# Optimization experiments

Hardware: AMD Instinct MI355X
Metric: run time of the kernel (lower is better)

Reference implementation:

```python
import jax, jax.numpy as jnp
import numpy as np

OBS_DIM = 256
ACTION_DIM = 4
NUM_OBJECTS = 16
HIDDEN = 512
BATCH = 4096
LN_EPS = 1e-5


def _uniform(key, shape, stdv):
    return jax.random.uniform(key, shape, jnp.float32, -stdv, stdv)


def setup_inputs() -> dict:
    key = jax.random.key(0)
    ks = jax.random.split(key, 8)
    node_in = OBS_DIM + ACTION_DIM
    s1 = 1.0 / np.sqrt(HIDDEN)
    s3 = 1.0 / np.sqrt(OBS_DIM)
    return {
        "states": jax.random.normal(ks[0], (BATCH, NUM_OBJECTS, OBS_DIM), jnp.float32),
        "action": jax.random.randint(ks[1], (BATCH,), 0, ACTION_DIM * NUM_OBJECTS, jnp.int64 if jax.config.jax_enable_x64 else jnp.int32),
        "W1": _uniform(ks[2], (node_in, HIDDEN), s1),
        "b1": _uniform(ks[3], (HIDDEN,), s1),
        "W2": _uniform(ks[4], (HIDDEN, HIDDEN), s1),
        "b2": _uniform(ks[5], (HIDDEN,), s1),
        "W3": _uniform(ks[6], (HIDDEN, OBS_DIM), s3),
        "b3": _uniform(ks[7], (OBS_DIM,), s3),
        "ln_g": jnp.ones((HIDDEN,), jnp.float32),
        "ln_b": jnp.zeros((HIDDEN,), jnp.float32),
    }


def _gc(x, W, b):
    # x: [B, O, d_in]. adj = block_diag(ones(O,O)/O) == per-graph mean pooling,
    # broadcast back to every node in the graph.
    s = jnp.einsum("bod,dh->boh", x, W)
    m = jnp.mean(s, axis=1, keepdims=True)  # [B, 1, h]
    return jnp.broadcast_to(m, s.shape) + b


def _layernorm(x, g, b):
    mu = jnp.mean(x, axis=-1, keepdims=True)
    var = jnp.mean(jnp.square(x - mu), axis=-1, keepdims=True)
    return (x - mu) * jax.lax.rsqrt(var + LN_EPS) * g + b


def reference(states, action, W1, b1, W2, b2, W3, b3, ln_g, ln_b):
    B, O, D = states.shape
    # one_hot(action, A*O).view(-1, A) == per-node one-hot slices
    a = jax.nn.one_hot(action, ACTION_DIM * O, dtype=states.dtype)
    a = a.reshape(B, O, ACTION_DIM)
    x = jnp.concatenate([states, a], axis=-1)  # [B, O, D+A]
    h = jax.nn.relu(_gc(x, W1, b1))
    h = jax.nn.relu(_layernorm(_gc(h, W2, b2), ln_g, ln_b))
    out = _gc(h, W3, b3)  # [B, O, obs_dim]
    return out
```

## Files before the change

kernel.cpp:

```cpp
#include <hip/hip_runtime.h>
#include <hip/hip_bf16.h>

#define BSZ   4096
#define NOBJ  16
#define DOBS  256
#define ADIM  4
#define HID   512
#define KP1   288

#define MB    16
#define XP1   296
#define HP    520
#define TP    260

typedef unsigned short u16;
typedef __bf16 bf16x8 __attribute__((ext_vector_type(8)));
typedef float  f32x4  __attribute__((ext_vector_type(4)));
typedef unsigned short u16x8 __attribute__((ext_vector_type(8)));

static __device__ __forceinline__ u16 f2bf(float f) {
    __hip_bfloat16 h = __float2bfloat16(f);
    return __builtin_bit_cast(u16, h);
}
static __device__ __forceinline__ bf16x8 ldg8(const u16* p) {
    return __builtin_bit_cast(bf16x8, *(const u16x8*)p);
}

__global__ void prep_weights(const float* __restrict__ W1, const float* __restrict__ W2,
                             const float* __restrict__ W3,
                             u16* __restrict__ W1T, u16* __restrict__ W2T, u16* __restrict__ W3T) {
    int idx = blockIdx.x * 256 + threadIdx.x;
    const int n1 = HID * KP1;
    const int n2 = HID * HID;
    const int n3 = DOBS * HID;
    if (idx < n1) {
        int h = idx / KP1, k = idx % KP1;
        float v = (k < DOBS + ADIM) ? W1[k * HID + h] : 0.0f;
        W1T[idx] = f2bf(v);
    } else if (idx < n1 + n2) {
        int t = idx - n1;
        int h = t / HID, k = t % HID;
        W2T[t] = f2bf(W2[k * HID + h]);
    } else if (idx < n1 + n2 + n3) {
        int t = idx - n1 - n2;
        int n = t / HID, k = t % HID;
        W3T[t] = f2bf(W3[k * DOBS + n]);
    }
}

__global__ __launch_bounds__(256) void fused_mlp(
    const float* __restrict__ states, const int* __restrict__ action,
    const u16* __restrict__ W1T, const float* __restrict__ b1,
    const u16* __restrict__ W2T, const float* __restrict__ b2,
    const u16* __restrict__ W3T, const float* __restrict__ b3,
    const float* __restrict__ lng, const float* __restrict__ lnb,
    float* __restrict__ out)
{
    __shared__ u16   xbar[MB][XP1];
    __shared__ u16   h1[MB][HP];
    __shared__ u16   h2[MB][HP];
    __shared__ float t3[MB][TP];
    __shared__ float red[2][4][MB];

    const int t  = threadIdx.x;
    const int w  = t >> 6;
    const int l  = t & 63;
    const int lr = l & 15;
    const int lg = l >> 4;
    const int b0 = blockIdx.x * MB;

    {
        const int d = t;
        #pragma unroll 4
        for (int r = 0; r < MB; ++r) {
            const float* sp = states + ((size_t)(b0 + r) * NOBJ) * DOBS + d;
            float s = 0.f;
            #pragma unroll
            for (int o = 0; o < NOBJ; ++o) s += sp[o * DOBS];
            xbar[r][d] = f2bf(s * (1.0f / NOBJ));
        }
        if (t < MB) {
            int a = action[b0 + t] & 3;
            #pragma unroll
            for (int k = 0; k < KP1 - DOBS; ++k)
                xbar[t][DOBS + k] = f2bf(k == a ? (1.0f / NOBJ) : 0.0f);
        }
    }
    __syncthreads();

    {
        f32x4 acc[8] = {};
        #pragma unroll 3
        for (int ks = 0; ks < KP1 / 32; ++ks) {
            bf16x8 a = ldg8(&xbar[lr][ks * 32 + lg * 8]);
            #pragma unroll
            for (int nb = 0; nb < 8; ++nb) {
                int n = w * 128 + nb * 16 + lr;
                bf16x8 bv = ldg8(W1T + (size_t)n * KP1 + ks * 32 + lg * 8);
                acc[nb] = __builtin_amdgcn_mfma_f32_16x16x32_bf16(a, bv, acc[nb], 0, 0, 0);
            }
        }
        #pragma unroll
        for (int nb = 0; nb < 8; ++nb) {
            int n = w * 128 + nb * 16 + lr;
            float bias = b1[n];
            #pragma unroll
            for (int r = 0; r < 4; ++r)
                h1[lg * 4 + r][n] = f2bf(fmaxf(acc[nb][r] + bias, 0.f));
        }
    }
    __syncthreads();

    {
        f32x4 acc[8] = {};
        #pragma unroll 4
        for (int ks = 0; ks < HID / 32; ++ks) {
            bf16x8 a = ldg8(&h1[lr][ks * 32 + lg * 8]);
            #pragma unroll
            for (int nb = 0; nb < 8; ++nb) {
                int n = w * 128 + nb * 16 + lr;
                bf16x8 bv = ldg8(W2T + (size_t)n * HID + ks * 32 + lg * 8);
                acc[nb] = __builtin_amdgcn_mfma_f32_16x16x32_bf16(a, bv, acc[nb], 0, 0, 0);
            }
        }
        float s1[4] = {0.f, 0.f, 0.f, 0.f}, s2[4] = {0.f, 0.f, 0.f, 0.f};
        #pragma unroll
        for (int nb = 0; nb < 8; ++nb) {
            float bias = b2[w * 128 + nb * 16 + lr];
            #pragma unroll
            for (int r = 0; r < 4; ++r) {
                float v = acc[nb][r] + bias;
                acc[nb][r] = v;
                s1[r] += v;
                s2[r] += v * v;
            }
        }
        #pragma unroll
        for (int r = 0; r < 4; ++r) {
            #pragma unroll
            for (int m = 8; m; m >>= 1) {
                s1[r] += __shfl_xor(s1[r], m, 64);
                s2[r] += __shfl_xor(s2[r], m, 64);
            }
            if (lr == 0) {
                red[0][w][lg * 4 + r] = s1[r];
                red[1][w][lg * 4 + r] = s2[r];
            }
        }
        __syncthreads();
        float muv[4], rsv[4];
        #pragma unroll
        for (int r = 0; r < 4; ++r) {
            int m = lg * 4 + r;
            float S1 = red[0][0][m] + red[0][1][m] + red[0][2][m] + red[0][3][m];
            float S2 = red[1][0][m] + red[1][1][m] + red[1][2][m] + red[1][3][m];
            float mu = S1 * (1.0f / HID);
            float var = S2 * (1.0f / HID) - mu * mu;
            muv[r] = mu;
            rsv[r] = rsqrtf(var + 1e-5f);
        }
        #pragma unroll
        for (int nb = 0; nb < 8; ++nb) {
            int n = w * 128 + nb * 16 + lr;
            float g = lng[n], bb = lnb[n];
            #pragma unroll
            for (int r = 0; r < 4; ++r) {
                float y = (acc[nb][r] - muv[r]) * rsv[r] * g + bb;
                h2[lg * 4 + r][n] = f2bf(fmaxf(y, 0.f));
            }
        }
    }
    __syncthreads();

    {
        f32x4 acc[4] = {};
        #pragma unroll 4
        for (int ks = 0; ks < HID / 32; ++ks) {
            bf16x8 a = ldg8(&h2[lr][ks * 32 + lg * 8]);
            #pragma unroll
            for (int nb = 0; nb < 4; ++nb) {
                int n = w * 64 + nb * 16 + lr;
                bf16x8 bv = ldg8(W3T + (size_t)n * HID + ks * 32 + lg * 8);
                acc[nb] = __builtin_amdgcn_mfma_f32_16x16x32_bf16(a, bv, acc[nb], 0, 0, 0);
            }
        }
        #pragma unroll
        for (int nb = 0; nb < 4; ++nb) {
            int n = w * 64 + nb * 16 + lr;
            float bias = b3[n];
            #pragma unroll
            for (int r = 0; r < 4; ++r)
                t3[lg * 4 + r][n] = acc[nb][r] + bias;
        }
    }
    __syncthreads();

    {
        #pragma unroll 4
        for (int i = 0; i < 64; ++i) {
            int flat = i * 256 + t;
            int d4 = flat & 63;
            int o  = (flat >> 6) & 15;
            int r  = flat >> 10;
            float4 v = *(const float4*)&t3[r][d4 * 4];
            *(float4*)(out + ((size_t)(b0 + r) * NOBJ + o) * DOBS + d4 * 4) = v;
        }
    }
}

extern "C" void kernel_launch(void* const* d_in, const int* in_sizes, int n_in,
                              void* d_out, int out_size, void* d_ws, size_t ws_size,
                              hipStream_t stream) {
    const float* states = (const float*)d_in[0];
    const int*   action = (const int*)d_in[1];
    const float* W1 = (const float*)d_in[2];
    const float* b1 = (const float*)d_in[3];
    const float* W2 = (const float*)d_in[4];
    const float* b2 = (const float*)d_in[5];
    const float* W3 = (const float*)d_in[6];
    const float* b3 = (const float*)d_in[7];
    const float* lng = (const float*)d_in[8];
    const float* lnb = (const float*)d_in[9];
    float* out = (float*)d_out;

    char* ws = (char*)d_ws;
    size_t off = 0;
    auto alloc = [&](size_t bytes) -> void* {
        void* p = ws + off;
        off = (off + bytes + 255) & ~(size_t)255;
        return p;
    };
    u16* W1T = (u16*)alloc((size_t)HID * KP1 * 2);
    u16* W2T = (u16*)alloc((size_t)HID * HID * 2);
    u16* W3T = (u16*)alloc((size_t)DOBS * HID * 2);

    prep_weights<<<2112, 256, 0, stream>>>(W1, W2, W3, W1T, W2T, W3T);
    fused_mlp<<<BSZ / MB, 256, 0, stream>>>(states, action,
                                            W1T, b1, W2T, b2, W3T, b3,
                                            lng, lnb, out);
}
```

Baseline: 161.3 us.

## Double block to 512 threads and vectorize states mean-pooling loads

Raises the fused kernel's block from 4 to 8 waves, so each wave computes half as many output columns in every GEMM stage and the LayerNorm reduction sums across 8 waves. The states mean pooling now uses float4 loads and writes four bf16 values at once. The aim is more parallelism and memory-level concurrency per block for the load-bound pooling and store phases, at the cost of larger blocks, which may lower the number of resident blocks per CU.

```diff
diff --git a/kernel.cpp b/kernel.cpp
--- a/kernel.cpp
+++ b/kernel.cpp
@@ -9,6 +9,7 @@
 #define KP1   288
 
 #define MB    16
+#define NT    512
 #define XP1   296
 #define HP    520
 #define TP    260
@@ -17,6 +18,7 @@
 typedef __bf16 bf16x8 __attribute__((ext_vector_type(8)));
 typedef float  f32x4  __attribute__((ext_vector_type(4)));
 typedef unsigned short u16x8 __attribute__((ext_vector_type(8)));
+typedef unsigned short u16x4 __attribute__((ext_vector_type(4)));
 
 static __device__ __forceinline__ u16 f2bf(float f) {
     __hip_bfloat16 h = __float2bfloat16(f);
@@ -48,7 +50,7 @@
     }
 }
 
-__global__ __launch_bounds__(256) void fused_mlp(
+__global__ __launch_bounds__(NT) void fused_mlp(
     const float* __restrict__ states, const int* __restrict__ action,
     const u16* __restrict__ W1T, const float* __restrict__ b1,
     const u16* __restrict__ W2T, const float* __restrict__ b2,
@@ -60,7 +62,7 @@
     __shared__ u16   h1[MB][HP];
     __shared__ u16   h2[MB][HP];
     __shared__ float t3[MB][TP];
-    __shared__ float red[2][4][MB];
+    __shared__ float red[2][8][MB];
 
     const int t  = threadIdx.x;
     const int w  = t >> 6;
@@ -70,14 +72,21 @@
     const int b0 = blockIdx.x * MB;
 
     {
-        const int d = t;
-        #pragma unroll 4
-        for (int r = 0; r < MB; ++r) {
-            const float* sp = states + ((size_t)(b0 + r) * NOBJ) * DOBS + d;
-            float s = 0.f;
-            #pragma unroll
-            for (int o = 0; o < NOBJ; ++o) s += sp[o * DOBS];
-            xbar[r][d] = f2bf(s * (1.0f / NOBJ));
+        const float4* sf4 = (const float4*)states;
+        #pragma unroll
+        for (int p = 0; p < 2; ++p) {
+            int idx = p * NT + t;
+            int r = idx >> 6, d4 = idx & 63;
+            float sx = 0.f, sy = 0.f, sz = 0.f, sw = 0.f;
+            const float4* rp = sf4 + (((size_t)(b0 + r) * NOBJ) << 6) + d4;
+            #pragma unroll
+            for (int o = 0; o < NOBJ; ++o) {
+                float4 v = rp[o << 6];
+                sx += v.x; sy += v.y; sz += v.z; sw += v.w;
+            }
+            u16x4 st = { f2bf(sx * (1.0f / NOBJ)), f2bf(sy * (1.0f / NOBJ)),
+                         f2bf(sz * (1.0f / NOBJ)), f2bf(sw * (1.0f / NOBJ)) };
+            *(u16x4*)&xbar[r][d4 * 4] = st;
         }
         if (t < MB) {
             int a = action[b0 + t] & 3;
@@ -89,20 +98,20 @@
     __syncthreads();
 
     {
-        f32x4 acc[8] = {};
+        f32x4 acc[4] = {};
         #pragma unroll 3
         for (int ks = 0; ks < KP1 / 32; ++ks) {
             bf16x8 a = ldg8(&xbar[lr][ks * 32 + lg * 8]);
             #pragma unroll
-            for (int nb = 0; nb < 8; ++nb) {
-                int n = w * 128 + nb * 16 + lr;
+            for (int nb = 0; nb < 4; ++nb) {
+                int n = w * 64 + nb * 16 + lr;
                 bf16x8 bv = ldg8(W1T + (size_t)n * KP1 + ks * 32 + lg * 8);
                 acc[nb] = __builtin_amdgcn_mfma_f32_16x16x32_bf16(a, bv, acc[nb], 0, 0, 0);
             }
         }
         #pragma unroll
-        for (int nb = 0; nb < 8; ++nb) {
-            int n = w * 128 + nb * 16 + lr;
+        for (int nb = 0; nb < 4; ++nb) {
+            int n = w * 64 + nb * 16 + lr;
             float bias = b1[n];
             #pragma unroll
             for (int r = 0; r < 4; ++r)
@@ -112,21 +121,21 @@
     __syncthreads();
 
     {
-        f32x4 acc[8] = {};
+        f32x4 acc[4] = {};
         #pragma unroll 4
         for (int ks = 0; ks < HID / 32; ++ks) {
             bf16x8 a = ldg8(&h1[lr][ks * 32 + lg * 8]);
             #pragma unroll
-            for (int nb = 0; nb < 8; ++nb) {
-                int n = w * 128 + nb * 16 + lr;
+            for (int nb = 0; nb < 4; ++nb) {
+                int n = w * 64 + nb * 16 + lr;
                 bf16x8 bv = ldg8(W2T + (size_t)n * HID + ks * 32 + lg * 8);
                 acc[nb] = __builtin_amdgcn_mfma_f32_16x16x32_bf16(a, bv, acc[nb], 0, 0, 0);
             }
         }
         float s1[4] = {0.f, 0.f, 0.f, 0.f}, s2[4] = {0.f, 0.f, 0.f, 0.f};
         #pragma unroll
-        for (int nb = 0; nb < 8; ++nb) {
-            float bias = b2[w * 128 + nb * 16 + lr];
+        for (int nb = 0; nb < 4; ++nb) {
+            float bias = b2[w * 64 + nb * 16 + lr];
             #pragma unroll
             for (int r = 0; r < 4; ++r) {
                 float v = acc[nb][r] + bias;
@@ -152,16 +161,17 @@
         #pragma unroll
         for (int r = 0; r < 4; ++r) {
             int m = lg * 4 + r;
-            float S1 = red[0][0][m] + red[0][1][m] + red[0][2][m] + red[0][3][m];
-            float S2 = red[1][0][m] + red[1][1][m] + red[1][2][m] + red[1][3][m];
+            float S1 = 0.f, S2 = 0.f;
+            #pragma unroll
+            for (int ww = 0; ww < 8; ++ww) { S1 += red[0][ww][m]; S2 += red[1][ww][m]; }
             float mu = S1 * (1.0f / HID);
             float var = S2 * (1.0f / HID) - mu * mu;
             muv[r] = mu;
             rsv[r] = rsqrtf(var + 1e-5f);
         }
         #pragma unroll
-        for (int nb = 0; nb < 8; ++nb) {
-            int n = w * 128 + nb * 16 + lr;
+        for (int nb = 0; nb < 4; ++nb) {
+            int n = w * 64 + nb * 16 + lr;
             float g = lng[n], bb = lnb[n];
             #pragma unroll
             for (int r = 0; r < 4; ++r) {
@@ -173,20 +183,20 @@
     __syncthreads();
 
     {
-        f32x4 acc[4] = {};
+        f32x4 acc[2] = {};
         #pragma unroll 4
         for (int ks = 0; ks < HID / 32; ++ks) {
             bf16x8 a = ldg8(&h2[lr][ks * 32 + lg * 8]);
             #pragma unroll
-            for (int nb = 0; nb < 4; ++nb) {
-                int n = w * 64 + nb * 16 + lr;
+            for (int nb = 0; nb < 2; ++nb) {
+                int n = w * 32 + nb * 16 + lr;
                 bf16x8 bv = ldg8(W3T + (size_t)n * HID + ks * 32 + lg * 8);
                 acc[nb] = __builtin_amdgcn_mfma_f32_16x16x32_bf16(a, bv, acc[nb], 0, 0, 0);
             }
         }
         #pragma unroll
-        for (int nb = 0; nb < 4; ++nb) {
-            int n = w * 64 + nb * 16 + lr;
+        for (int nb = 0; nb < 2; ++nb) {
+            int n = w * 32 + nb * 16 + lr;
             float bias = b3[n];
             #pragma unroll
             for (int r = 0; r < 4; ++r)
@@ -196,9 +206,9 @@
     __syncthreads();
 
     {
-        #pragma unroll 4
-        for (int i = 0; i < 64; ++i) {
-            int flat = i * 256 + t;
+        #pragma unroll 8
+        for (int i = 0; i < 32; ++i) {
+            int flat = i * NT + t;
             int d4 = flat & 63;
             int o  = (flat >> 6) & 15;
             int r  = flat >> 10;
@@ -235,7 +245,7 @@
     u16* W3T = (u16*)alloc((size_t)DOBS * HID * 2);
 
     prep_weights<<<2112, 256, 0, stream>>>(W1, W2, W3, W1T, W2T, W3T);
-    fused_mlp<<<BSZ / MB, 256, 0, stream>>>(states, action,
-                                            W1T, b1, W2T, b2, W3T, b3,
-                                            lng, lnb, out);
-}
+    fused_mlp<<<BSZ / MB, NT, 0, stream>>>(states, action,
+                                           W1T, b1, W2T, b2, W3T, b3,
+                                           lng, lnb, out);
+}
```

Result: no change. 158.9 us (-1.5%).
